# Optimization experiments

Measured on AMD Instinct MI355X. Metric: run time of the kernel, lower is better.

The kernel has to match this reference:

```python
import jax, jax.numpy as jnp
import numpy as np


def _maxpool2x2(t):
    # t: [B, C, H, W] -> [B, C, H//2, W//2]
    B, C, H, W = t.shape
    return t.reshape(B, C, H // 2, 2, W // 2, 2).max(axis=(3, 5))


def setup_inputs() -> dict:
    key = jax.random.key(0)
    ks = jax.random.split(key, 6)
    B, C, H, W = 2, 64, 128, 128
    x = jax.random.normal(ks[0], (B, C, H, W), dtype=jnp.float32)
    w_theta = jax.random.normal(ks[1], (C // 8, C), dtype=jnp.float32) * 0.05
    w_phi = jax.random.normal(ks[2], (C // 8, C), dtype=jnp.float32) * 0.05
    w_g = jax.random.normal(ks[3], (C // 2, C), dtype=jnp.float32) * 0.05
    w_o = jax.random.normal(ks[4], (C, C // 2), dtype=jnp.float32) * 0.05
    gamma = jnp.ones((1,), dtype=jnp.float32)
    return {"x": x, "w_theta": w_theta, "w_phi": w_phi, "w_g": w_g,
            "w_o": w_o, "gamma": gamma}


def reference(x, w_theta, w_phi, w_g, w_o, gamma):
    B, C, H, W = x.shape
    N = H * W            # query length
    M = (H // 2) * (W // 2)  # downsampled key/value length

    # conv1x1 projections (kernel_size=1 == per-pixel matmul over channels)
    theta = jnp.einsum('bchw,oc->bohw', x, w_theta).reshape(B, C // 8, N)
    phi = jnp.einsum('bchw,oc->bohw', x, w_phi)
    phi = _maxpool2x2(phi).reshape(B, C // 8, M)

    # attention: [B, N, M], unscaled dot product + softmax over keys
    attn = jax.nn.softmax(jnp.einsum('bdn,bdm->bnm', theta, phi), axis=-1)

    g = jnp.einsum('bchw,oc->bohw', x, w_g)
    g = _maxpool2x2(g).reshape(B, C // 2, M)

    attn_g = jnp.einsum('bcm,bnm->bcn', g, attn).reshape(B, C // 2, H, W)
    attn_g = jnp.einsum('bchw,oc->bohw', attn_g, w_o)
    return x + gamma * attn_g
```

## Files before the change

### kernel.cpp

```cpp
#include <hip/hip_runtime.h>

#define BB 2
#define CC 64
#define HH 128
#define WW 128
#define NN (HH*WW)
#define MM ((HH/2)*(WW/2))
#define CV 32
#define LOG2E 1.44269504088896f

typedef __attribute__((ext_vector_type(8))) short bf16x8;
typedef __attribute__((ext_vector_type(4))) float f32x4;
typedef unsigned int uint32;

union U8 { bf16x8 v; uint32 u[4]; };

__device__ __forceinline__ short f2bf(float f) {
    union { float f; unsigned u; } v; v.f = f;
    unsigned u = v.u + 0x7fffu + ((v.u >> 16) & 1u);
    return (short)(u >> 16);
}
__device__ __forceinline__ uint32 pack2bf(float lo, float hi) {
    return (uint32)(unsigned short)f2bf(lo) | ((uint32)(unsigned short)f2bf(hi) << 16);
}
__device__ __forceinline__ uint32 packperm(float lo, float hi) {
    union { float f; uint32 u; } a, b; a.f = lo; b.f = hi;
    return __builtin_amdgcn_perm(b.u, a.u, 0x07060302u);
}
__device__ __forceinline__ void gl_lds16(const short* g, short* l) {
    __builtin_amdgcn_global_load_lds(
        (const __attribute__((address_space(1))) void*)g,
        (__attribute__((address_space(3))) void*)l, 16, 0, 0);
}

__global__ __launch_bounds__(256, 4) void proj_kernel(
    const float* __restrict__ x, const float* __restrict__ wt,
    const float* __restrict__ wp, const float* __restrict__ wg,
    short* __restrict__ Qb, short* __restrict__ Kb, short* __restrict__ Vt)
{
    __shared__ float plds[8192];
    __shared__ float phi_lds[512];
    int tid = threadIdx.x;
    int px = tid & 63, part = tid >> 6;
    int sb = blockIdx.x >> 2, cq = blockIdx.x & 3;
    int b = blockIdx.y, z = blockIdx.z;
    int row = px >> 5, col = cq*32 + (px & 31);
    int n = (2*sb + row)*WW + col;
    int wbase = __builtin_amdgcn_readfirstlane(part*16);

    float xv[16];
    #pragma unroll
    for (int i = 0; i < 16; ++i)
        xv[i] = x[((b*CC + part*16 + i) << 14) + n];

    if (z == 0) {
        float po[16];
        #pragma unroll
        for (int o = 0; o < 8; ++o) {
            float a = 0.f;
            #pragma unroll
            for (int i = 0; i < 16; ++i) a += wt[o*64 + wbase + i]*xv[i];
            po[o] = a;
        }
        #pragma unroll
        for (int o = 0; o < 8; ++o) {
            float a = 0.f;
            #pragma unroll
            for (int i = 0; i < 16; ++i) a += wp[o*64 + wbase + i]*xv[i];
            po[8+o] = a;
        }
        #pragma unroll
        for (int o = 0; o < 16; ++o) plds[(o*4 + part)*64 + px] = po[o];
        __syncthreads();
        int og = tid >> 6;
        float sm[4];
        #pragma unroll
        for (int j = 0; j < 4; ++j) {
            int o = og*4 + j;
            sm[j] = (plds[(o*4+0)*64+px] + plds[(o*4+1)*64+px])
                  + (plds[(o*4+2)*64+px] + plds[(o*4+3)*64+px]);
        }
        if (og < 2) {
            uint2 val;
            val.x = pack2bf(sm[0]*LOG2E, sm[1]*LOG2E);
            val.y = pack2bf(sm[2]*LOG2E, sm[3]*LOG2E);
            ((uint2*)Qb)[(b*NN + n)*2 + og] = val;
        } else {
            #pragma unroll
            for (int j = 0; j < 4; ++j)
                phi_lds[((og-2)*4 + j)*64 + px] = sm[j];
        }
        __syncthreads();
        if (tid < 128) {
            int mm = tid & 15, ch = tid >> 4;
            int p00 = 2*mm, p01 = p00+1, p10 = 32+2*mm, p11 = p10+1;
            float mx = fmaxf(fmaxf(phi_lds[ch*64+p00], phi_lds[ch*64+p01]),
                             fmaxf(phi_lds[ch*64+p10], phi_lds[ch*64+p11]));
            int m = sb*64 + cq*16 + mm;
            Kb[(b*MM + m)*8 + ch] = f2bf(mx);
        }
    } else {
        float po[32];
        #pragma unroll
        for (int o = 0; o < 32; ++o) {
            float a = 0.f;
            #pragma unroll
            for (int i = 0; i < 16; ++i) a += wg[o*64 + wbase + i]*xv[i];
            po[o] = a;
        }
        #pragma unroll
        for (int o = 0; o < 32; ++o) plds[(o*4 + part)*64 + px] = po[o];
        __syncthreads();
        int og = tid >> 6;
        float sm[8];
        #pragma unroll
        for (int j = 0; j < 8; ++j) {
            int o = og*8 + j;
            sm[j] = (plds[(o*4+0)*64+px] + plds[(o*4+1)*64+px])
                  + (plds[(o*4+2)*64+px] + plds[(o*4+3)*64+px]);
        }
        __syncthreads();
        #pragma unroll
        for (int j = 0; j < 8; ++j)
            plds[(og*8 + j)*64 + px] = sm[j];
        __syncthreads();
        int mm = tid & 15, chb = tid >> 4;
        int p00 = 2*mm, p01 = p00+1, p10 = 32+2*mm, p11 = p10+1;
        int w64 = cq*16 + mm;
        int hh = w64 >> 5, w = w64 & 31;
        int slot = ((w >> 2) & 3)*8 + (w & 3) + ((w >> 4) << 2);
        int pos64 = hh*32 + slot;
        #pragma unroll
        for (int j = 0; j < 2; ++j) {
            int ch = chb*2 + j;
            float mx = fmaxf(fmaxf(plds[ch*64+p00], plds[ch*64+p01]),
                             fmaxf(plds[ch*64+p10], plds[ch*64+p11]));
            int colv = (pos64 >> 3) ^ (ch & 7);
            Vt[(b*CV + ch)*MM + sb*64 + colv*8 + (pos64 & 7)] = f2bf(mx);
        }
    }
}

__global__ __launch_bounds__(512, 4) void attn_kernel(
    const short* __restrict__ Qb, const short* __restrict__ Kb,
    const short* __restrict__ Vt, const float* __restrict__ x,
    const float* __restrict__ wo, const float* __restrict__ gamma,
    float* __restrict__ out)
{
    __shared__ short ldsK[2][4][512];
    __shared__ short ldsV[2][4][2048];
    __shared__ float comb[2][2][576];
    int tid = threadIdx.x;
    int wave = tid >> 6, lane = tid & 63;
    int quad = lane >> 4, c15 = lane & 15, sw = c15 & 7;
    int qtr = wave >> 1, qpair = wave & 1;
    int blk = blockIdx.x;
    int b = blk >> 8;
    int qblk = (blk & 255)*64;
    int q0 = qblk + qpair*32;

    const f32x4 zero4 = {0.f, 0.f, 0.f, 0.f};
    bf16x8 zero8 = (bf16x8)0;
    U8 ones; ones.u[0] = ones.u[1] = ones.u[2] = ones.u[3] = 0x3F803F80u;

    bf16x8 bq0 = (quad == 0) ? ((const bf16x8*)Qb)[b*NN + q0 + c15]      : zero8;
    bf16x8 bq1 = (quad == 0) ? ((const bf16x8*)Qb)[b*NN + q0 + 16 + c15] : zero8;

    const short* vsrcA = Vt + ((size_t)(b*CV + 16*qpair + (lane >> 3)))*MM
                       + qtr*1024 + (lane & 7)*8;
    const short* vsrcB = vsrcA + 8*MM;
    const short* ksrc  = Kb + (size_t)b*MM*8 + (qtr*1024 + lane)*8;
    short* vdstA[2] = { &ldsV[0][qtr][qpair*1024 + lane*8],
                        &ldsV[1][qtr][qpair*1024 + lane*8] };
    short* vdstB[2] = { vdstA[0] + 512, vdstA[1] + 512 };
    short* kdst[2]  = { &ldsK[0][qtr][lane*8], &ldsK[1][qtr][lane*8] };

    {
        gl_lds16(vsrcA, vdstA[0]);
        gl_lds16(vsrcB, vdstB[0]);
        if (qpair == 0) gl_lds16(ksrc, kdst[0]);
    }
    __syncthreads();

    f32x4 D0A = zero4, D1A = zero4, DlA = zero4;
    f32x4 D0B = zero4, D1B = zero4, DlB = zero4;

    for (int sc = 0; sc < 16; ++sc) {
        int scn = (sc + 1 > 15) ? 15 : sc + 1;
        int nb = (sc + 1) & 1;
        gl_lds16(vsrcA + scn*64, vdstA[nb]);
        gl_lds16(vsrcB + scn*64, vdstB[nb]);
        if (qpair == 0) gl_lds16(ksrc + scn*512, kdst[nb]);

        const short* bk = ldsK[sc & 1][qtr];
        const short* bv = ldsV[sc & 1][qtr];
        #pragma unroll
        for (int h = 0; h < 2; ++h) {
            bf16x8 kf0 = *(const bf16x8*)(bk + (h*32 + c15)*8);
            bf16x8 kf1 = *(const bf16x8*)(bk + (h*32 + 16 + c15)*8);
            int col8 = ((h*4 + quad) ^ sw)*8;
            bf16x8 a0 = *(const bf16x8*)(bv + c15*64 + col8);
            bf16x8 a1 = *(const bf16x8*)(bv + (16 + c15)*64 + col8);
            f32x4 s0A = __builtin_amdgcn_mfma_f32_16x16x32_bf16(kf0, bq0, zero4, 0, 0, 0);
            f32x4 s1A = __builtin_amdgcn_mfma_f32_16x16x32_bf16(kf1, bq0, zero4, 0, 0, 0);
            f32x4 s0B = __builtin_amdgcn_mfma_f32_16x16x32_bf16(kf0, bq1, zero4, 0, 0, 0);
            f32x4 s1B = __builtin_amdgcn_mfma_f32_16x16x32_bf16(kf1, bq1, zero4, 0, 0, 0);
            U8 bpA, bpB;
            bpA.u[0] = packperm(__builtin_amdgcn_exp2f(s0A[0]), __builtin_amdgcn_exp2f(s0A[1]));
            bpA.u[1] = packperm(__builtin_amdgcn_exp2f(s0A[2]), __builtin_amdgcn_exp2f(s0A[3]));
            bpA.u[2] = packperm(__builtin_amdgcn_exp2f(s1A[0]), __builtin_amdgcn_exp2f(s1A[1]));
            bpA.u[3] = packperm(__builtin_amdgcn_exp2f(s1A[2]), __builtin_amdgcn_exp2f(s1A[3]));
            bpB.u[0] = packperm(__builtin_amdgcn_exp2f(s0B[0]), __builtin_amdgcn_exp2f(s0B[1]));
            bpB.u[1] = packperm(__builtin_amdgcn_exp2f(s0B[2]), __builtin_amdgcn_exp2f(s0B[3]));
            bpB.u[2] = packperm(__builtin_amdgcn_exp2f(s1B[0]), __builtin_amdgcn_exp2f(s1B[1]));
            bpB.u[3] = packperm(__builtin_amdgcn_exp2f(s1B[2]), __builtin_amdgcn_exp2f(s1B[3]));
            D0A = __builtin_amdgcn_mfma_f32_16x16x32_bf16(a0, bpA.v, D0A, 0, 0, 0);
            D1A = __builtin_amdgcn_mfma_f32_16x16x32_bf16(a1, bpA.v, D1A, 0, 0, 0);
            DlA = __builtin_amdgcn_mfma_f32_16x16x32_bf16(ones.v, bpA.v, DlA, 0, 0, 0);
            D0B = __builtin_amdgcn_mfma_f32_16x16x32_bf16(a0, bpB.v, D0B, 0, 0, 0);
            D1B = __builtin_amdgcn_mfma_f32_16x16x32_bf16(a1, bpB.v, D1B, 0, 0, 0);
            DlB = __builtin_amdgcn_mfma_f32_16x16x32_bf16(ones.v, bpB.v, DlB, 0, 0, 0);
        }
        __syncthreads();
    }

    #pragma unroll
    for (int r = 1; r < 4; ++r) {
        if (qtr == r) {
            float* cA = &comb[qpair][0][lane*9];
            cA[0]=D0A[0]; cA[1]=D0A[1]; cA[2]=D0A[2]; cA[3]=D0A[3];
            cA[4]=D1A[0]; cA[5]=D1A[1]; cA[6]=D1A[2]; cA[7]=D1A[3];
            cA[8]=DlA[0];
            float* cB = &comb[qpair][1][lane*9];
            cB[0]=D0B[0]; cB[1]=D0B[1]; cB[2]=D0B[2]; cB[3]=D0B[3];
            cB[4]=D1B[0]; cB[5]=D1B[1]; cB[6]=D1B[2]; cB[7]=D1B[3];
            cB[8]=DlB[0];
        }
        __syncthreads();
        if (qtr == 0) {
            const float* cA = &comb[qpair][0][lane*9];
            D0A[0]+=cA[0]; D0A[1]+=cA[1]; D0A[2]+=cA[2]; D0A[3]+=cA[3];
            D1A[0]+=cA[4]; D1A[1]+=cA[5]; D1A[2]+=cA[6]; D1A[3]+=cA[7];
            DlA[0]+=cA[8];
            const float* cB = &comb[qpair][1][lane*9];
            D0B[0]+=cB[0]; D0B[1]+=cB[1]; D0B[2]+=cB[2]; D0B[3]+=cB[3];
            D1B[0]+=cB[4]; D1B[1]+=cB[5]; D1B[2]+=cB[6]; D1B[3]+=cB[7];
            DlB[0]+=cB[8];
        }
        __syncthreads();
    }
    if (qtr != 0) return;

    float rlA = 1.0f / DlA[0];
    float rlB = 1.0f / DlB[0];
    U8 ByA, ByB;
    ByA.u[0] = pack2bf(D0A[0]*rlA, D0A[1]*rlA); ByA.u[1] = pack2bf(D0A[2]*rlA, D0A[3]*rlA);
    ByA.u[2] = pack2bf(D1A[0]*rlA, D1A[1]*rlA); ByA.u[3] = pack2bf(D1A[2]*rlA, D1A[3]*rlA);
    ByB.u[0] = pack2bf(D0B[0]*rlB, D0B[1]*rlB); ByB.u[1] = pack2bf(D0B[2]*rlB, D0B[3]*rlB);
    ByB.u[2] = pack2bf(D1B[0]*rlB, D1B[1]*rlB); ByB.u[3] = pack2bf(D1B[2]*rlB, D1B[3]*rlB);

    float gam = gamma[0];
    #pragma unroll
    for (int t = 0; t < 4; ++t) {
        int co = t*16 + c15;
        float4 wlo = *(const float4*)(wo + co*32 + quad*4);
        float4 whi = *(const float4*)(wo + co*32 + 16 + quad*4);
        U8 aw;
        aw.u[0] = pack2bf(wlo.x, wlo.y); aw.u[1] = pack2bf(wlo.z, wlo.w);
        aw.u[2] = pack2bf(whi.x, whi.y); aw.u[3] = pack2bf(whi.z, whi.w);
        f32x4 oA = __builtin_amdgcn_mfma_f32_16x16x32_bf16(aw.v, ByA.v, zero4, 0, 0, 0);
        f32x4 oB = __builtin_amdgcn_mfma_f32_16x16x32_bf16(aw.v, ByB.v, zero4, 0, 0, 0);
        #pragma unroll
        for (int r2 = 0; r2 < 4; ++r2) {
            int co_r = t*16 + quad*4 + r2;
            int base = ((b*CC + co_r) << 14) + q0 + c15;
            out[base]      = x[base]      + gam*oA[r2];
            out[base + 16] = x[base + 16] + gam*oB[r2];
        }
    }
}

extern "C" void kernel_launch(void* const* d_in, const int* in_sizes, int n_in,
                              void* d_out, int out_size, void* d_ws, size_t ws_size,
                              hipStream_t stream) {
    const float* x     = (const float*)d_in[0];
    const float* wt    = (const float*)d_in[1];
    const float* wp    = (const float*)d_in[2];
    const float* wg    = (const float*)d_in[3];
    const float* wo    = (const float*)d_in[4];
    const float* gamma = (const float*)d_in[5];
    float* out = (float*)d_out;

    char* ws = (char*)d_ws;
    short* Qb = (short*)(ws);
    short* Kb = (short*)(ws + 524288);
    short* Vt = (short*)(ws + 655360);

    dim3 g1(256, BB, 2);
    proj_kernel<<<g1, 256, 0, stream>>>(x, wt, wp, wg, Qb, Kb, Vt);
    attn_kernel<<<BB*NN/64, 512, 0, stream>>>(Qb, Kb, Vt, x, wo, gamma, out);
}
```

Before: 99.38 us.

## Make attention waves load private K/V slices and drop per-chunk block barriers

The attention kernel now launches 256-thread blocks covering 32 queries, and each wave handles one quarter of the keys. Every wave loads its own K and full V slice into LDS, so the two query-pair waves no longer share loads. The per-chunk __syncthreads is replaced by explicit vmcnt waits on the async global-to-LDS copies. The cross-wave combine buffer now reuses ldsV instead of a separate array. This removes block-wide barriers from the main loop but doubles global K/V traffic per query and relies on the waves touching only their own LDS region, with each wave waiting on its own outstanding loads.

```diff
diff --git a/kernel.cpp b/kernel.cpp
--- a/kernel.cpp
+++ b/kernel.cpp
@@ -141,7 +141,7 @@
     }
 }
 
-__global__ __launch_bounds__(512, 4) void attn_kernel(
+__global__ __launch_bounds__(256, 4) void attn_kernel(
     const short* __restrict__ Qb, const short* __restrict__ Kb,
     const short* __restrict__ Vt, const float* __restrict__ x,
     const float* __restrict__ wo, const float* __restrict__ gamma,
@@ -149,15 +149,12 @@
 {
     __shared__ short ldsK[2][4][512];
     __shared__ short ldsV[2][4][2048];
-    __shared__ float comb[2][2][576];
     int tid = threadIdx.x;
-    int wave = tid >> 6, lane = tid & 63;
+    int qtr = tid >> 6, lane = tid & 63;
     int quad = lane >> 4, c15 = lane & 15, sw = c15 & 7;
-    int qtr = wave >> 1, qpair = wave & 1;
     int blk = blockIdx.x;
-    int b = blk >> 8;
-    int qblk = (blk & 255)*64;
-    int q0 = qblk + qpair*32;
+    int b = blk >> 9;
+    int q0 = (blk & 511)*32;
 
     const f32x4 zero4 = {0.f, 0.f, 0.f, 0.f};
     bf16x8 zero8 = (bf16x8)0;
@@ -166,34 +163,46 @@
     bf16x8 bq0 = (quad == 0) ? ((const bf16x8*)Qb)[b*NN + q0 + c15]      : zero8;
     bf16x8 bq1 = (quad == 0) ? ((const bf16x8*)Qb)[b*NN + q0 + 16 + c15] : zero8;
 
-    const short* vsrcA = Vt + ((size_t)(b*CV + 16*qpair + (lane >> 3)))*MM
+    const short* ksrc  = Kb + (size_t)b*MM*8 + (qtr*1024 + lane)*8;
+    const short* vsrcA = Vt + ((size_t)(b*CV + (lane >> 3)))*MM
                        + qtr*1024 + (lane & 7)*8;
     const short* vsrcB = vsrcA + 8*MM;
-    const short* ksrc  = Kb + (size_t)b*MM*8 + (qtr*1024 + lane)*8;
-    short* vdstA[2] = { &ldsV[0][qtr][qpair*1024 + lane*8],
-                        &ldsV[1][qtr][qpair*1024 + lane*8] };
-    short* vdstB[2] = { vdstA[0] + 512, vdstA[1] + 512 };
-    short* kdst[2]  = { &ldsK[0][qtr][lane*8], &ldsK[1][qtr][lane*8] };
+    const short* vsrcC = vsrcA + 16*MM;
+    const short* vsrcD = vsrcA + 24*MM;
+    short* kd0 = &ldsK[0][qtr][lane*8];
+    short* kd1 = &ldsK[1][qtr][lane*8];
+    short* vd0 = &ldsV[0][qtr][lane*8];
+    short* vd1 = &ldsV[1][qtr][lane*8];
 
     {
-        gl_lds16(vsrcA, vdstA[0]);
-        gl_lds16(vsrcB, vdstB[0]);
-        if (qpair == 0) gl_lds16(ksrc, kdst[0]);
-    }
-    __syncthreads();
+        gl_lds16(vsrcA, vd0);
+        gl_lds16(vsrcB, vd0 + 512);
+        gl_lds16(vsrcC, vd0 + 1024);
+        gl_lds16(vsrcD, vd0 + 1536);
+        gl_lds16(ksrc, kd0);
+    }
 
     f32x4 D0A = zero4, D1A = zero4, DlA = zero4;
     f32x4 D0B = zero4, D1B = zero4, DlB = zero4;
 
     for (int sc = 0; sc < 16; ++sc) {
-        int scn = (sc + 1 > 15) ? 15 : sc + 1;
-        int nb = (sc + 1) & 1;
-        gl_lds16(vsrcA + scn*64, vdstA[nb]);
-        gl_lds16(vsrcB + scn*64, vdstB[nb]);
-        if (qpair == 0) gl_lds16(ksrc + scn*512, kdst[nb]);
-
-        const short* bk = ldsK[sc & 1][qtr];
-        const short* bv = ldsV[sc & 1][qtr];
+        if (sc < 15) {
+            int scn = sc + 1;
+            short* vd = (scn & 1) ? vd1 : vd0;
+            short* kd = (scn & 1) ? kd1 : kd0;
+            gl_lds16(vsrcA + scn*64, vd);
+            gl_lds16(vsrcB + scn*64, vd + 512);
+            gl_lds16(vsrcC + scn*64, vd + 1024);
+            gl_lds16(vsrcD + scn*64, vd + 1536);
+            gl_lds16(ksrc + scn*512, kd);
+            asm volatile("s_waitcnt vmcnt(5)" ::: "memory");
+        } else {
+            asm volatile("s_waitcnt vmcnt(0)" ::: "memory");
+        }
+        __builtin_amdgcn_sched_barrier(0);
+
+        const short* bk = (sc & 1) ? &ldsK[1][qtr][0] : &ldsK[0][qtr][0];
+        const short* bv = (sc & 1) ? &ldsV[1][qtr][0] : &ldsV[0][qtr][0];
         #pragma unroll
         for (int h = 0; h < 2; ++h) {
             bf16x8 kf0 = *(const bf16x8*)(bk + (h*32 + c15)*8);
@@ -221,28 +230,27 @@
             D1B = __builtin_amdgcn_mfma_f32_16x16x32_bf16(a1, bpB.v, D1B, 0, 0, 0);
             DlB = __builtin_amdgcn_mfma_f32_16x16x32_bf16(ones.v, bpB.v, DlB, 0, 0, 0);
         }
-        __syncthreads();
     }
 
     #pragma unroll
     for (int r = 1; r < 4; ++r) {
         if (qtr == r) {
-            float* cA = &comb[qpair][0][lane*9];
+            float* cA = (float*)&ldsV[0][r][0] + lane*9;
             cA[0]=D0A[0]; cA[1]=D0A[1]; cA[2]=D0A[2]; cA[3]=D0A[3];
             cA[4]=D1A[0]; cA[5]=D1A[1]; cA[6]=D1A[2]; cA[7]=D1A[3];
             cA[8]=DlA[0];
-            float* cB = &comb[qpair][1][lane*9];
+            float* cB = (float*)&ldsV[1][r][0] + lane*9;
             cB[0]=D0B[0]; cB[1]=D0B[1]; cB[2]=D0B[2]; cB[3]=D0B[3];
             cB[4]=D1B[0]; cB[5]=D1B[1]; cB[6]=D1B[2]; cB[7]=D1B[3];
             cB[8]=DlB[0];
         }
         __syncthreads();
         if (qtr == 0) {
-            const float* cA = &comb[qpair][0][lane*9];
+            const float* cA = (const float*)&ldsV[0][r][0] + lane*9;
             D0A[0]+=cA[0]; D0A[1]+=cA[1]; D0A[2]+=cA[2]; D0A[3]+=cA[3];
             D1A[0]+=cA[4]; D1A[1]+=cA[5]; D1A[2]+=cA[6]; D1A[3]+=cA[7];
             DlA[0]+=cA[8];
-            const float* cB = &comb[qpair][1][lane*9];
+            const float* cB = (const float*)&ldsV[1][r][0] + lane*9;
             D0B[0]+=cB[0]; D0B[1]+=cB[1]; D0B[2]+=cB[2]; D0B[3]+=cB[3];
             D1B[0]+=cB[4]; D1B[1]+=cB[5]; D1B[2]+=cB[6]; D1B[3]+=cB[7];
             DlB[0]+=cB[8];
@@ -298,5 +306,5 @@
 
     dim3 g1(256, BB, 2);
     proj_kernel<<<g1, 256, 0, stream>>>(x, wt, wp, wg, Qb, Kb, Vt);
-    attn_kernel<<<BB*NN/64, 512, 0, stream>>>(Qb, Kb, Vt, x, wo, gamma, out);
-}
+    attn_kernel<<<BB*NN/32, 256, 0, stream>>>(Qb, Kb, Vt, x, wo, gamma, out);
+}
```

New measurement: 100.1 us, median of 2. Within noise of the previous version (+0.7%).
